# Performance work log

Hardware: AMD Instinct MI355X
Metric: run time of the kernel (lower is better)

## Reference

```python
import jax, jax.numpy as jnp
import numpy as np
from jax import lax

DIM = 128
DEPTH = 2
OUT_DIM = 256
DIM_HEAD = 64
HEADS = 8
WS = 16
INNER = DIM_HEAD * HEADS
EPS = 1e-5
SCALE = DIM_HEAD ** (-0.5)


def setup_inputs() -> dict:
    key = jax.random.key(0)
    ks = jax.random.split(key, 20)
    s = 0.02
    L = DEPTH
    inp = {
        "x": jax.random.normal(ks[0], (1, DIM, 256, 256), dtype=jnp.float32),
        "ln1_g": jnp.ones((L, DIM), dtype=jnp.float32),
        "ln1_b": jnp.zeros((L, DIM), dtype=jnp.float32),
        "wq": jax.random.normal(ks[1], (L, INNER, DIM), dtype=jnp.float32) * s,
        "wkv": jax.random.normal(ks[2], (L, 2 * INNER, DIM), dtype=jnp.float32) * s,
        "wo": jax.random.normal(ks[3], (L, DIM, INNER), dtype=jnp.float32) * s,
        "bo": jnp.zeros((L, DIM), dtype=jnp.float32),
        "ln2_g": jnp.ones((L, DIM), dtype=jnp.float32),
        "ln2_b": jnp.zeros((L, DIM), dtype=jnp.float32),
        "w_in": jax.random.normal(ks[4], (L, DIM, DIM), dtype=jnp.float32) * s,
        "b_in": jnp.zeros((L, DIM), dtype=jnp.float32),
        "w_c3": jax.random.normal(ks[5], (L, OUT_DIM, DIM, 3, 3), dtype=jnp.float32) * s,
        "b_c3": jnp.zeros((L, OUT_DIM), dtype=jnp.float32),
        "w_c1": jax.random.normal(ks[6], (L, DIM, OUT_DIM), dtype=jnp.float32) * s,
        "b_c1": jnp.zeros((L, DIM), dtype=jnp.float32),
        "w_outer": jax.random.normal(ks[7], (DIM, DIM), dtype=jnp.float32) * s,
        "b_outer": jnp.zeros((DIM,), dtype=jnp.float32),
    }
    return inp


def _layernorm(x, g, b):
    # channel-wise (dim=1) norm; note torch code uses (std + eps), not sqrt(var + eps)
    mean = jnp.mean(x, axis=1, keepdims=True)
    std = jnp.sqrt(jnp.var(x, axis=1, keepdims=True))
    return (x - mean) / (std + EPS) * g[None, :, None, None] + b[None, :, None, None]


def _conv1x1(w, x, b=None):
    y = jnp.einsum('oi,bihw->bohw', w, x)
    if b is not None:
        y = y + b[None, :, None, None]
    return y


def _to_windows(t, B, H, W):
    # [B, HEADS*DIM_HEAD, H, W] -> [B*HEADS*nx*ny, WS*WS, DIM_HEAD]
    nx, ny = H // WS, W // WS
    t = t.reshape(B, HEADS, DIM_HEAD, nx, WS, ny, WS)
    t = t.transpose(0, 1, 3, 5, 4, 6, 2)
    return t.reshape(B * HEADS * nx * ny, WS * WS, DIM_HEAD)


def _from_windows(t, B, H, W):
    nx, ny = H // WS, W // WS
    t = t.reshape(B, HEADS, nx, ny, WS, WS, DIM_HEAD)
    t = t.transpose(0, 1, 6, 2, 4, 3, 5)
    return t.reshape(B, HEADS * DIM_HEAD, H, W)


def _attention(x, wq_l, wkv_l, wo_l, bo_l):
    B, _, H, W = x.shape
    q = _conv1x1(wq_l, x)
    kv = _conv1x1(wkv_l, x)
    k, v = kv[:, :INNER], kv[:, INNER:]
    q = _to_windows(q, B, H, W)
    k = _to_windows(k, B, H, W)
    v = _to_windows(v, B, H, W)
    sim = jnp.einsum('bid,bjd->bij', q, k) * SCALE  # [nwin, 256, 256]
    attn = jax.nn.softmax(sim, axis=-1)
    out = jnp.einsum('bij,bjd->bid', attn, v)
    out = _from_windows(out, B, H, W)
    return _conv1x1(wo_l, out, bo_l)


def _feedforward(x, w_in_l, b_in_l, w_c3_l, b_c3_l, w_c1_l, b_c1_l):
    h = _conv1x1(w_in_l, x, b_in_l)
    h = lax.conv_general_dilated(h, w_c3_l, window_strides=(1, 1), padding='SAME',
                                 dimension_numbers=('NCHW', 'OIHW', 'NCHW'))
    h = h + b_c3_l[None, :, None, None]
    h = jax.nn.gelu(h, approximate=False)
    return _conv1x1(w_c1_l, h, b_c1_l)


def reference(x, ln1_g, ln1_b, wq, wkv, wo, bo, ln2_g, ln2_b,
              w_in, b_in, w_c3, b_c3, w_c1, b_c1, w_outer, b_outer):
    for l in range(DEPTH):
        xn = _layernorm(x, ln1_g[l], ln1_b[l])
        x = _attention(xn, wq[l], wkv[l], wo[l], bo[l]) + x
        xn = _layernorm(x, ln2_g[l], ln2_b[l])
        x = _feedforward(xn, w_in[l], b_in[l], w_c3[l], b_c3[l], w_c1[l], b_c1[l]) + x
    return _conv1x1(w_outer, x, b_outer) + x
```

## Files before the change

kernel.cpp:

```cpp
#include <hip/hip_runtime.h>
#include <hip/hip_bf16.h>
#include <math.h>

typedef __hip_bfloat16 bf16;
typedef float f4 __attribute__((ext_vector_type(4)));
typedef short s8 __attribute__((ext_vector_type(8)));
typedef unsigned int u2 __attribute__((ext_vector_type(2)));
typedef unsigned int u4v __attribute__((ext_vector_type(4)));

__device__ __forceinline__ void gload16(const void* g, char* l) {
  __builtin_amdgcn_global_load_lds(
      (const __attribute__((address_space(1))) unsigned int*)g,
      (__attribute__((address_space(3))) unsigned int*)l, 16, 0, 0);
}
__device__ __forceinline__ unsigned short bfr(float f) {
  bf16 h = __float2bfloat16(f);
  return *(unsigned short*)&h;
}
__device__ __forceinline__ unsigned int pk2(float a, float b) {
  return (unsigned int)bfr(a) | ((unsigned int)bfr(b) << 16);
}
__device__ __forceinline__ unsigned int pkt(float a, float b) {
  return __builtin_amdgcn_perm(__float_as_uint(b), __float_as_uint(a), 0x07060302u);
}

__global__ __launch_bounds__(256) void prep_w(
    const float* __restrict__ wq, const float* __restrict__ wkv,
    const float* __restrict__ wo, const float* __restrict__ win,
    const float* __restrict__ wc3, const float* __restrict__ wc1,
    const float* __restrict__ wout, ushort* __restrict__ cw)
{
  int i = blockIdx.x * 256 + threadIdx.x;
  float v;
  if (i < 131072) v = wq[i];
  else if (i < 393216) v = wkv[i - 131072];
  else if (i < 524288) v = wo[i - 393216];
  else if (i < 1146880) return;
  else if (i < 1212416) v = wc1[i - 1146880];
  else if (i < 1228800) v = wout[i - 1212416];
  else if (i < 1230848) { cw[i] = 0; return; }
  else return;
  cw[i] = bfr(v);
}

__global__ __launch_bounds__(128) void prep_fold(
    const float* __restrict__ wc3, const float* __restrict__ win,
    const float* __restrict__ b_in, ushort* __restrict__ cw3out,
    float* __restrict__ T)
{
  __shared__ float col[128][9];
  __shared__ float sred[2][9];
  const int lyr = blockIdx.x >> 8, m = blockIdx.x & 255;
  const int tid = threadIdx.x;
  const float* src = wc3 + (((size_t)lyr * 256 + m) * 128 + tid) * 9;
#pragma unroll
  for (int t = 0; t < 9; ++t) col[tid][t] = src[t];
  float bi = b_in[lyr * 128 + tid];
  float sb[9];
#pragma unroll
  for (int t = 0; t < 9; ++t) {
    float v = col[tid][t] * bi;
    v += __shfl_xor(v, 1, 64);  v += __shfl_xor(v, 2, 64);
    v += __shfl_xor(v, 4, 64);  v += __shfl_xor(v, 8, 64);
    v += __shfl_xor(v, 16, 64); v += __shfl_xor(v, 32, 64);
    sb[t] = v;
  }
  if ((tid & 63) == 0) {
#pragma unroll
    for (int t = 0; t < 9; ++t) sred[tid >> 6][t] = sb[t];
  }
  __syncthreads();
  float acc[9] = {0.f,0.f,0.f,0.f,0.f,0.f,0.f,0.f,0.f};
  const float* wrow = win + (size_t)lyr * 16384 + tid;
  for (int c = 0; c < 128; ++c) {
    float wv = wrow[(size_t)c * 128];
#pragma unroll
    for (int t = 0; t < 9; ++t) acc[t] += col[c][t] * wv;
  }
  ushort* dst = cw3out + (size_t)lyr * 294912 + (size_t)m * 1152 + tid;
#pragma unroll
  for (int t = 0; t < 9; ++t) dst[t * 128] = bfr(acc[t]);
  if (tid == 0) {
    float s[9];
#pragma unroll
    for (int t = 0; t < 9; ++t) s[t] = sred[0][t] + sred[1][t];
    float* Tl = T + lyr * 2304;
    Tl[0 * 256 + m] = s[0]+s[1]+s[2]+s[3]+s[4]+s[5]+s[6]+s[7]+s[8];
    Tl[1 * 256 + m] = s[0] + s[1] + s[2];
    Tl[2 * 256 + m] = s[6] + s[7] + s[8];
    Tl[3 * 256 + m] = s[0] + s[3] + s[6];
    Tl[4 * 256 + m] = s[2] + s[5] + s[8];
    Tl[5 * 256 + m] = s[0];
    Tl[6 * 256 + m] = s[2];
    Tl[7 * 256 + m] = s[6];
    Tl[8 * 256 + m] = s[8];
  }
}

template<bool NCHW>
__global__ __launch_bounds__(256) void ln_nhwc(
    const float* __restrict__ x, const float* __restrict__ g,
    const float* __restrict__ b, ushort* __restrict__ y)
{
  const int p = blockIdx.x * 256 + threadIdx.x;
  f4 v[32];
  float s = 0.f, s2 = 0.f;
  if constexpr (NCHW) {
#pragma unroll
    for (int i = 0; i < 32; ++i)
#pragma unroll
      for (int j = 0; j < 4; ++j) {
        float t = x[(size_t)(i * 4 + j) * 65536 + p];
        v[i][j] = t; s += t; s2 += t * t;
      }
  } else {
    const f4* base = (const f4*)(x + (size_t)p * 128);
#pragma unroll
    for (int i = 0; i < 32; ++i) {
      v[i] = base[i];
#pragma unroll
      for (int j = 0; j < 4; ++j) { s += v[i][j]; s2 += v[i][j] * v[i][j]; }
    }
  }
  float mean = s * (1.f / 128.f);
  float var = s2 * (1.f / 128.f) - mean * mean;
  var = var > 0.f ? var : 0.f;
  float inv = 1.f / (sqrtf(var) + 1e-5f);
  u2* dst = (u2*)(y + (size_t)p * 128);
#pragma unroll
  for (int i = 0; i < 32; ++i) {
    f4 gg = *(const f4*)(g + i * 4);
    f4 bb = *(const f4*)(b + i * 4);
    float f0 = (v[i][0] - mean) * inv * gg[0] + bb[0];
    float f1 = (v[i][1] - mean) * inv * gg[1] + bb[1];
    float f2 = (v[i][2] - mean) * inv * gg[2] + bb[2];
    float f3 = (v[i][3] - mean) * inv * gg[3] + bb[3];
    u2 st; st.x = pk2(f0, f1); st.y = pk2(f2, f3);
    dst[i] = st;
  }
}

template<int MODE>
__global__ __launch_bounds__(256) void gemm_nhwc(
    const ushort* __restrict__ A, const ushort* __restrict__ X,
    const float* __restrict__ bias, const float* __restrict__ res,
    void* __restrict__ out, ushort* __restrict__ out2,
    const ushort* __restrict__ A2,
    const float* __restrict__ lng, const float* __restrict__ lnb,
    ushort* __restrict__ xn, const int K, const int M)
{
  constexpr unsigned SMSZ = (MODE == 7) ? 65536u : 32768u;
  __shared__ __align__(16) char sm[SMSZ];
  const int tid = threadIdx.x, w = tid >> 6, l = tid & 63;
  const int quad = l >> 4, l15 = l & 15;
  const int n0 = blockIdx.x * 128, m0 = blockIdx.y * 128;
  const int mh = (w & 1) * 64, nh = (w >> 1) * 64;
  const f4 fz = {0.f, 0.f, 0.f, 0.f};
  f4 acc[4][4];
#pragma unroll
  for (int a = 0; a < 4; ++a)
#pragma unroll
    for (int b2 = 0; b2 < 4; ++b2) acc[a][b2] = fz;

  const int KI = K >> 6;
  for (int kk = 0; kk < KI; ++kk) {
    if (kk) __syncthreads();
    const int k0 = kk << 6;
#pragma unroll
    for (int j = 0; j < 4; ++j) {
      int p = j * 256 + tid, r = p >> 3, c = (p & 7) ^ (r & 7);
      gload16(A + (size_t)(m0 + r) * K + k0 + c * 8, sm + (j * 256 + w * 64) * 16);
    }
#pragma unroll
    for (int j = 0; j < 4; ++j) {
      int p = j * 256 + tid, r = p >> 3, c = (p & 7) ^ (r & 7);
      gload16(X + (size_t)(n0 + r) * K + k0 + c * 8, sm + 16384 + (j * 256 + w * 64) * 16);
    }
    __syncthreads();
#pragma unroll
    for (int ks = 0; ks < 2; ++ks) {
      s8 af[4], bx[4];
#pragma unroll
      for (int mt = 0; mt < 4; ++mt) {
        int rr = mh + mt * 16 + l15;
        af[mt] = *(const s8*)(sm + rr * 128 + (((ks * 4 + quad) ^ (rr & 7)) << 4));
      }
#pragma unroll
      for (int nt = 0; nt < 4; ++nt) {
        int rr = nh + nt * 16 + l15;
        bx[nt] = *(const s8*)(sm + 16384 + rr * 128 + (((ks * 4 + quad) ^ (rr & 7)) << 4));
      }
#pragma unroll
      for (int mt = 0; mt < 4; ++mt)
#pragma unroll
        for (int nt = 0; nt < 4; ++nt)
          acc[mt][nt] = __builtin_amdgcn_mfma_f32_16x16x32_bf16(af[mt], bx[nt], acc[mt][nt], 0, 0, 0);
    }
  }

  if constexpr (MODE == 7) {
#pragma unroll
    for (int mt = 0; mt < 4; ++mt) {
      const int m = mh + mt * 16 + quad * 4;
      f4 bb = *(const f4*)(bias + m);
      const int seg = m >> 6, kl = m & 63;
#pragma unroll
      for (int nt = 0; nt < 4; ++nt) {
        const int r = nh + nt * 16 + l15;
        f4 v = acc[mt][nt] + bb + *(const f4*)(res + (size_t)(n0 + r) * 128 + m);
        acc[mt][nt] = v;
        u2 st; st.x = pk2(v[0], v[1]); st.y = pk2(v[2], v[3]);
        *(u2*)(sm + 32768 + seg * 16384 + r * 128 +
               (((kl >> 3) ^ (r & 7)) << 4) + (kl & 7) * 2) = st;
      }
    }
    __syncthreads();
#pragma unroll
    for (int kk2 = 0; kk2 < 2; ++kk2)
#pragma unroll
      for (int j = 0; j < 4; ++j) {
        int p = j * 256 + tid, r = p >> 3, c = (p & 7) ^ (r & 7);
        gload16(A2 + (size_t)r * 128 + kk2 * 64 + c * 8,
                sm + kk2 * 16384 + (j * 256 + w * 64) * 16);
      }
    __syncthreads();
    f4 acc2[4][4];
#pragma unroll
    for (int a = 0; a < 4; ++a)
#pragma unroll
      for (int b2 = 0; b2 < 4; ++b2) acc2[a][b2] = fz;
#pragma unroll
    for (int kk2 = 0; kk2 < 2; ++kk2)
#pragma unroll
      for (int ks = 0; ks < 2; ++ks) {
        s8 af[4], bx[4];
#pragma unroll
        for (int mt = 0; mt < 4; ++mt) {
          int rr = mh + mt * 16 + l15;
          af[mt] = *(const s8*)(sm + kk2 * 16384 + rr * 128 + (((ks * 4 + quad) ^ (rr & 7)) << 4));
        }
#pragma unroll
        for (int nt = 0; nt < 4; ++nt) {
          int rr = nh + nt * 16 + l15;
          bx[nt] = *(const s8*)(sm + 32768 + kk2 * 16384 + rr * 128 + (((ks * 4 + quad) ^ (rr & 7)) << 4));
        }
#pragma unroll
        for (int mt = 0; mt < 4; ++mt)
#pragma unroll
          for (int nt = 0; nt < 4; ++nt)
            acc2[mt][nt] = __builtin_amdgcn_mfma_f32_16x16x32_bf16(af[mt], bx[nt], acc2[mt][nt], 0, 0, 0);
      }
#pragma unroll
    for (int mt = 0; mt < 4; ++mt) {
      const int m = mh + mt * 16 + quad * 4;
      f4 bo2 = *(const f4*)(lng + m);
#pragma unroll
      for (int nt = 0; nt < 4; ++nt) {
        const int n = n0 + nh + nt * 16 + l15;
        f4 v2 = acc2[mt][nt] + bo2 + acc[mt][nt];
#pragma unroll
        for (int i = 0; i < 4; ++i)
          ((float*)out)[(size_t)(m + i) * 65536 + n] = v2[i];
      }
    }
    return;
  }

  if constexpr (MODE == 5 || MODE == 6) {
    float s1[4] = {0.f, 0.f, 0.f, 0.f}, s2[4] = {0.f, 0.f, 0.f, 0.f};
#pragma unroll
    for (int mt = 0; mt < 4; ++mt) {
      const int m = mh + mt * 16 + quad * 4;
      f4 bb = *(const f4*)(bias + m);
#pragma unroll
      for (int nt = 0; nt < 4; ++nt) {
        const int n = n0 + nh + nt * 16 + l15;
        f4 v = acc[mt][nt] + bb;
        if constexpr (MODE == 5) {
          f4 r = *(const f4*)(res + (size_t)n * 128 + m);
          v += r;
        } else {
          f4 r;
#pragma unroll
          for (int i = 0; i < 4; ++i) r[i] = res[(size_t)(m + i) * 65536 + n];
          v += r;
        }
        *(f4*)((float*)out + (size_t)n * 128 + m) = v;
        acc[mt][nt] = v;
        s1[nt] += v[0] + v[1] + v[2] + v[3];
        s2[nt] += v[0] * v[0] + v[1] * v[1] + v[2] * v[2] + v[3] * v[3];
      }
    }
    __syncthreads();
    float* pb = (float*)sm;
#pragma unroll
    for (int nt = 0; nt < 4; ++nt) {
      float a1 = s1[nt], a2 = s2[nt];
      a1 += __shfl_xor(a1, 16, 64); a1 += __shfl_xor(a1, 32, 64);
      a2 += __shfl_xor(a2, 16, 64); a2 += __shfl_xor(a2, 32, 64);
      s1[nt] = a1; s2[nt] = a2;
      if (quad == 0) {
        int pn = nh + nt * 16 + l15;
        pb[((w & 1) * 128 + pn) * 2]     = a1;
        pb[((w & 1) * 128 + pn) * 2 + 1] = a2;
      }
    }
    __syncthreads();
#pragma unroll
    for (int nt = 0; nt < 4; ++nt) {
      int pn = nh + nt * 16 + l15;
      float t1 = s1[nt] + pb[((1 - (w & 1)) * 128 + pn) * 2];
      float t2 = s2[nt] + pb[((1 - (w & 1)) * 128 + pn) * 2 + 1];
      float mean = t1 * (1.f / 128.f);
      float var = t2 * (1.f / 128.f) - mean * mean;
      var = var > 0.f ? var : 0.f;
      s1[nt] = mean;
      s2[nt] = 1.f / (sqrtf(var) + 1e-5f);
    }
#pragma unroll
    for (int mt = 0; mt < 4; ++mt) {
      const int m = mh + mt * 16 + quad * 4;
      f4 gg = *(const f4*)(lng + m);
      f4 b2 = *(const f4*)(lnb + m);
#pragma unroll
      for (int nt = 0; nt < 4; ++nt) {
        const int n = n0 + nh + nt * 16 + l15;
        f4 v = acc[mt][nt];
        float mean = s1[nt], inv = s2[nt];
        float f0 = (v[0] - mean) * inv * gg[0] + b2[0];
        float f1 = (v[1] - mean) * inv * gg[1] + b2[1];
        float f2 = (v[2] - mean) * inv * gg[2] + b2[2];
        float f3 = (v[3] - mean) * inv * gg[3] + b2[3];
        u2 st; st.x = pk2(f0, f1); st.y = pk2(f2, f3);
        *(u2*)(xn + (size_t)n * 128 + m) = st;
      }
    }
    return;
  }

#pragma unroll
  for (int mt = 0; mt < 4; ++mt) {
#pragma unroll
    for (int nt = 0; nt < 4; ++nt) {
      const int m = m0 + mh + mt * 16 + quad * 4;
      const int n = n0 + nh + nt * 16 + l15;
      f4 bb = *(const f4*)(bias + m);
      f4 v = acc[mt][nt] + bb;
      if constexpr (MODE == 0) {
        u2 st; st.x = pk2(v[0], v[1]); st.y = pk2(v[2], v[3]);
        *(u2*)((ushort*)out + (size_t)n * M + m) = st;
      } else if constexpr (MODE == 1 || MODE == 3) {
        f4 r = *(const f4*)(res + (size_t)n * M + m);
        v += r;
        *(f4*)((float*)out + (size_t)n * M + m) = v;
        if constexpr (MODE == 3) {
          u2 st; st.x = pk2(v[0], v[1]); st.y = pk2(v[2], v[3]);
          *(u2*)(out2 + (size_t)n * M + m) = st;
        }
      } else if constexpr (MODE == 4) {
        f4 r;
#pragma unroll
        for (int i = 0; i < 4; ++i) r[i] = res[(size_t)(m + i) * 65536 + n];
        v += r;
        *(f4*)((float*)out + (size_t)n * M + m) = v;
      } else {
        f4 r = *(const f4*)(res + (size_t)n * M + m);
#pragma unroll
        for (int i = 0; i < 4; ++i)
          ((float*)out)[(size_t)(m + i) * 65536 + n] = v[i] + r[i];
      }
    }
  }
}

__global__ __launch_bounds__(256) void conv3_kernel(
    const ushort* __restrict__ A, const ushort* __restrict__ X,
    const float* __restrict__ bias, ushort* __restrict__ out,
    const ushort* __restrict__ zp, const float* __restrict__ T)
{
  __shared__ __align__(16) char sm[32768];
  const int tid = threadIdx.x, w = tid >> 6, l = tid & 63;
  const int quad = l >> 4, l15 = l & 15;
  const int n0 = blockIdx.x * 128, m0 = blockIdx.y * 128;
  const int mh = (w & 1) * 64, nh = (w >> 1) * 64;
  const f4 fz = {0.f, 0.f, 0.f, 0.f};
  f4 acc[4][4];
#pragma unroll
  for (int a = 0; a < 4; ++a)
#pragma unroll
    for (int b2 = 0; b2 < 4; ++b2) acc[a][b2] = fz;

  for (int kk = 0; kk < 18; ++kk) {
    if (kk) __syncthreads();
    const int tap = kk >> 1, ky = tap / 3, kx = tap - ky * 3;
    const int dn = (ky - 1) * 256 + (kx - 1);
    const int kseg = (kk & 1) << 6;
#pragma unroll
    for (int j = 0; j < 4; ++j) {
      int p = j * 256 + tid, r = p >> 3, c = (p & 7) ^ (r & 7);
      gload16(A + (size_t)(m0 + r) * 1152 + kk * 64 + c * 8, sm + (j * 256 + w * 64) * 16);
    }
#pragma unroll
    for (int j = 0; j < 4; ++j) {
      int p = j * 256 + tid, r = p >> 3, c = (p & 7) ^ (r & 7);
      int nl = n0 + r;
      int ys = (nl >> 8) + ky - 1, xs = (nl & 255) + kx - 1;
      const ushort* gp = ((unsigned)ys < 256u && (unsigned)xs < 256u)
                         ? X + (size_t)(nl + dn) * 128 + kseg + c * 8 : zp;
      gload16(gp, sm + 16384 + (j * 256 + w * 64) * 16);
    }
    __syncthreads();
#pragma unroll
    for (int ks = 0; ks < 2; ++ks) {
      s8 af[4], bx[4];
#pragma unroll
      for (int mt = 0; mt < 4; ++mt) {
        int rr = mh + mt * 16 + l15;
        af[mt] = *(const s8*)(sm + rr * 128 + (((ks * 4 + quad) ^ (rr & 7)) << 4));
      }
#pragma unroll
      for (int nt = 0; nt < 4; ++nt) {
        int rr = nh + nt * 16 + l15;
        bx[nt] = *(const s8*)(sm + 16384 + rr * 128 + (((ks * 4 + quad) ^ (rr & 7)) << 4));
      }
#pragma unroll
      for (int mt = 0; mt < 4; ++mt)
#pragma unroll
        for (int nt = 0; nt < 4; ++nt)
          acc[mt][nt] = __builtin_amdgcn_mfma_f32_16x16x32_bf16(af[mt], bx[nt], acc[mt][nt], 0, 0, 0);
    }
  }
  const int y = n0 >> 8;
  const bool y0 = (y == 0), y1 = (y == 255);
  const int xbase = (n0 & 255) + nh;
#pragma unroll
  for (int mt = 0; mt < 4; ++mt) {
    const int m = m0 + mh + mt * 16 + quad * 4;
    f4 base = *(const f4*)(bias + m) + *(const f4*)(T + m);
    f4 Lc = *(const f4*)(T + 3 * 256 + m);
    f4 Rc = *(const f4*)(T + 4 * 256 + m);
    if (y0) {
      base -= *(const f4*)(T + 1 * 256 + m);
      Lc -= *(const f4*)(T + 5 * 256 + m);
      Rc -= *(const f4*)(T + 6 * 256 + m);
    }
    if (y1) {
      base -= *(const f4*)(T + 2 * 256 + m);
      Lc -= *(const f4*)(T + 7 * 256 + m);
      Rc -= *(const f4*)(T + 8 * 256 + m);
    }
#pragma unroll
    for (int nt = 0; nt < 4; ++nt) {
      const int n = n0 + nh + nt * 16 + l15;
      const int x = xbase + nt * 16 + l15;
      float fx0 = (x == 0) ? 1.f : 0.f;
      float fx1 = (x == 255) ? 1.f : 0.f;
      f4 v = acc[mt][nt] + base - Lc * fx0 - Rc * fx1;
      float g0 = 0.5f * v[0] * (1.f + erff(v[0] * 0.70710678118f));
      float g1 = 0.5f * v[1] * (1.f + erff(v[1] * 0.70710678118f));
      float g2 = 0.5f * v[2] * (1.f + erff(v[2] * 0.70710678118f));
      float g3 = 0.5f * v[3] * (1.f + erff(v[3] * 0.70710678118f));
      u2 st; st.x = pk2(g0, g1); st.y = pk2(g2, g3);
      *(u2*)(out + (size_t)n * 256 + m) = st;
    }
  }
}

__global__ __launch_bounds__(1024) void attn_kernel(
    const ushort* __restrict__ xn, const ushort* __restrict__ wq,
    const ushort* __restrict__ wkv, ushort* __restrict__ ao)
{
  __shared__ __align__(16) char sm[147456];
  const int tid = threadIdx.x, w = tid >> 6, l = tid & 63;
  const int quad = l >> 4, l15 = l & 15;
  const int win = blockIdx.x, head = blockIdx.y;
  const int nbase = ((win >> 4) << 12) + ((win & 15) << 4);
  char* RX  = sm;
  char* RW  = sm + 65536;
  char* RK  = sm + 114688;
  char* RVT = sm;
  char* Pw  = sm + 32768 + w * 2048;
  char* RO  = RW;
  const f4 fz = {0.f, 0.f, 0.f, 0.f};
  const int tokw = w * 16 + l15;

#pragma unroll
  for (int j = 0; j < 4; ++j) {
    int p = j * 1024 + tid, r = p >> 4, c = (p & 15) ^ (r & 15);
    int n = nbase + ((r >> 4) << 8) + (r & 15);
    gload16(xn + (size_t)n * 128 + c * 8, RX + (j * 1024 + w * 64) * 16);
  }
  {
    const ushort* wpq = wq + (size_t)head * 64 * 128;
    const ushort* wpk = wkv + (size_t)head * 64 * 128;
    const ushort* wpv = wkv + (size_t)(512 + head * 64) * 128;
    int r = tid >> 4, c = (tid & 15) ^ (r & 15);
    gload16(wpq + (size_t)r * 128 + c * 8, RW + w * 1024);
    gload16(wpk + (size_t)r * 128 + c * 8, RW + 16384 + w * 1024);
    gload16(wpv + (size_t)r * 128 + c * 8, RW + 32768 + w * 1024);
  }
  __syncthreads();

  s8 bq[2];
  {
    f4 acc[4];
#pragma unroll
    for (int a = 0; a < 4; ++a) acc[a] = fz;
#pragma unroll
    for (int ks = 0; ks < 4; ++ks) {
      s8 af[4], bx;
#pragma unroll
      for (int mt = 0; mt < 4; ++mt) {
        int rr = mt * 16 + l15;
        af[mt] = *(const s8*)(RW + rr * 256 + (((ks * 4 + quad) ^ (rr & 15)) << 4));
      }
      bx = *(const s8*)(RX + tokw * 256 + (((ks * 4 + quad) ^ (tokw & 15)) << 4));
#pragma unroll
      for (int mt = 0; mt < 4; ++mt)
        acc[mt] = __builtin_amdgcn_mfma_f32_16x16x32_bf16(af[mt], bx, acc[mt], 0, 0, 0);
    }
    unsigned pd[4][2];
#pragma unroll
    for (int mt = 0; mt < 4; ++mt) {
      pd[mt][0] = pkt(acc[mt][0], acc[mt][1]);
      pd[mt][1] = pkt(acc[mt][2], acc[mt][3]);
    }
#pragma unroll
    for (int ks = 0; ks < 2; ++ks) {
      u4v t;
#pragma unroll
      for (int dj = 0; dj < 4; ++dj) {
        int srcl = l15 + (((quad & 1) * 2 + (dj >> 1)) << 4);
        unsigned va = (unsigned)__shfl((int)pd[2 * ks][dj & 1], srcl, 64);
        unsigned vb = (unsigned)__shfl((int)pd[2 * ks + 1][dj & 1], srcl, 64);
        t[dj] = (quad < 2) ? va : vb;
      }
      bq[ks] = __builtin_bit_cast(s8, t);
    }
  }

  {
    f4 acc[4];
#pragma unroll
    for (int a = 0; a < 4; ++a) acc[a] = fz;
#pragma unroll
    for (int ks = 0; ks < 4; ++ks) {
      s8 af[4], bx;
#pragma unroll
      for (int mt = 0; mt < 4; ++mt) {
        int rr = mt * 16 + l15;
        af[mt] = *(const s8*)(RW + 16384 + rr * 256 + (((ks * 4 + quad) ^ (rr & 15)) << 4));
      }
      bx = *(const s8*)(RX + tokw * 256 + (((ks * 4 + quad) ^ (tokw & 15)) << 4));
#pragma unroll
      for (int mt = 0; mt < 4; ++mt)
        acc[mt] = __builtin_amdgcn_mfma_f32_16x16x32_bf16(af[mt], bx, acc[mt], 0, 0, 0);
    }
#pragma unroll
    for (int mt = 0; mt < 4; ++mt) {
      int d0 = mt * 16 + quad * 4;
      char* a = RK + tokw * 128 + (((d0 >> 3) ^ (tokw & 7)) << 4) + (d0 & 7) * 2;
      *(unsigned int*)a = pkt(acc[mt][0], acc[mt][1]);
      *(unsigned int*)(a + 4) = pkt(acc[mt][2], acc[mt][3]);
    }
  }

  {
    f4 acc[4];
#pragma unroll
    for (int a = 0; a < 4; ++a) acc[a] = fz;
#pragma unroll
    for (int ks = 0; ks < 4; ++ks) {
      s8 ax, bw[4];
      ax = *(const s8*)(RX + tokw * 256 + (((ks * 4 + quad) ^ (tokw & 15)) << 4));
#pragma unroll
      for (int nt = 0; nt < 4; ++nt) {
        int rr = nt * 16 + l15;
        bw[nt] = *(const s8*)(RW + 32768 + rr * 256 + (((ks * 4 + quad) ^ (rr & 15)) << 4));
      }
#pragma unroll
      for (int nt = 0; nt < 4; ++nt)
        acc[nt] = __builtin_amdgcn_mfma_f32_16x16x32_bf16(ax, bw[nt], acc[nt], 0, 0, 0);
    }
    __syncthreads();
#pragma unroll
    for (int nt = 0; nt < 4; ++nt) {
      int d = nt * 16 + l15, t0 = w * 16 + quad * 4;
      char* a = RVT + d * 512 + (((t0 >> 3) ^ (d & 31)) << 4) + (t0 & 7) * 2;
      *(unsigned int*)a = pkt(acc[nt][0], acc[nt][1]);
      *(unsigned int*)(a + 4) = pkt(acc[nt][2], acc[nt][3]);
    }
  }
  __syncthreads();

  f4 o[4];
  float lsum = 0.f;
#pragma unroll
  for (int a = 0; a < 4; ++a) o[a] = fz;

  for (int jt = 0; jt < 4; ++jt) {
    f4 s[4];
#pragma unroll
    for (int a = 0; a < 4; ++a) s[a] = fz;
#pragma unroll
    for (int ks = 0; ks < 2; ++ks) {
      s8 af[4];
#pragma unroll
      for (int mt = 0; mt < 4; ++mt) {
        int rr = jt * 64 + mt * 16 + l15;
        af[mt] = *(const s8*)(RK + rr * 128 + (((ks * 4 + quad) ^ (rr & 7)) << 4));
      }
      __builtin_amdgcn_s_setprio(1);
#pragma unroll
      for (int mt = 0; mt < 4; ++mt)
        s[mt] = __builtin_amdgcn_mfma_f32_16x16x32_bf16(af[mt], bq[ks], s[mt], 0, 0, 0);
      __builtin_amdgcn_s_setprio(0);
    }
#pragma unroll
    for (int mt = 0; mt < 4; ++mt) {
      float p0 = exp2f(s[mt][0] * 0.18033688f);
      float p1 = exp2f(s[mt][1] * 0.18033688f);
      float p2 = exp2f(s[mt][2] * 0.18033688f);
      float p3 = exp2f(s[mt][3] * 0.18033688f);
      lsum += p0 + p1 + p2 + p3;
      int j0 = mt * 16 + quad * 4;
      char* a = Pw + l15 * 128 + (((j0 >> 3) ^ (l15 & 7)) << 4) + (j0 & 7) * 2;
      *(unsigned int*)a = pkt(p0, p1);
      *(unsigned int*)(a + 4) = pkt(p2, p3);
    }
#pragma unroll
    for (int ks = 0; ks < 2; ++ks) {
      s8 av[4], bp;
#pragma unroll
      for (int mt = 0; mt < 4; ++mt) {
        int d = mt * 16 + l15;
        av[mt] = *(const s8*)(RVT + d * 512 + (((jt * 8 + ks * 4 + quad) ^ (d & 31)) << 4));
      }
      bp = *(const s8*)(Pw + l15 * 128 + (((ks * 4 + quad) ^ (l15 & 7)) << 4));
      __builtin_amdgcn_s_setprio(1);
#pragma unroll
      for (int mt = 0; mt < 4; ++mt)
        o[mt] = __builtin_amdgcn_mfma_f32_16x16x32_bf16(av[mt], bp, o[mt], 0, 0, 0);
      __builtin_amdgcn_s_setprio(0);
    }
  }

  float lv = lsum;
  lv += __shfl_xor(lv, 16, 64);
  lv += __shfl_xor(lv, 32, 64);
  const float inv = 1.f / lv;
#pragma unroll
  for (int mt = 0; mt < 4; ++mt) {
    int i = w * 16 + l15, d0 = mt * 16 + quad * 4;
    char* a = RO + i * 128 + (((d0 >> 3) ^ (i & 7)) << 4) + (d0 & 7) * 2;
    *(unsigned int*)a = pkt(o[mt][0] * inv, o[mt][1] * inv);
    *(unsigned int*)(a + 4) = pkt(o[mt][2] * inv, o[mt][3] * inv);
  }
  __syncthreads();
  const int tok = tid >> 2, q2 = tid & 3;
  const int n = nbase + ((tok >> 4) << 8) + (tok & 15);
  ushort* dst = ao + (size_t)n * 512 + head * 64;
#pragma unroll
  for (int c = 0; c < 2; ++c) {
    int chunk = q2 * 2 + c;
    u4v v = *(const u4v*)(RO + tok * 128 + ((chunk ^ (tok & 7)) << 4));
    *(u4v*)(dst + chunk * 8) = v;
  }
}

extern "C" void kernel_launch(void* const* d_in, const int* in_sizes, int n_in,
                              void* d_out, int out_size, void* d_ws, size_t ws_size,
                              hipStream_t stream)
{
  const float* x_in    = (const float*)d_in[0];
  const float* ln1_g   = (const float*)d_in[1];
  const float* ln1_b   = (const float*)d_in[2];
  const float* wq      = (const float*)d_in[3];
  const float* wkv     = (const float*)d_in[4];
  const float* wo      = (const float*)d_in[5];
  const float* bo      = (const float*)d_in[6];
  const float* ln2_g   = (const float*)d_in[7];
  const float* ln2_b   = (const float*)d_in[8];
  const float* w_in    = (const float*)d_in[9];
  const float* b_in    = (const float*)d_in[10];
  const float* w_c3    = (const float*)d_in[11];
  const float* b_c3    = (const float*)d_in[12];
  const float* w_c1    = (const float*)d_in[13];
  const float* b_c1    = (const float*)d_in[14];
  const float* w_outer = (const float*)d_in[15];
  const float* b_outer = (const float*)d_in[16];

  char* wsb = (char*)d_ws;
  ushort* CW = (ushort*)wsb;
  float*  TB = (float*)(wsb + 3145728);
  float*  XH = (float*)(wsb + 4194304);
  ushort* XN = (ushort*)(wsb + 37748736);
  ushort* AO = (ushort*)(wsb + 54525952);
  ushort* G  = (ushort*)(wsb + 138412032);

  const ushort* zp = CW + 1228800;
  dim3 b256(256);

  prep_w<<<dim3(4808), b256, 0, stream>>>(wq, wkv, wo, w_in, w_c3, w_c1, w_outer, CW);
  prep_fold<<<dim3(512), dim3(128), 0, stream>>>(w_c3, w_in, b_in, CW + 557056, TB);

  ln_nhwc<true><<<dim3(256), b256, 0, stream>>>(x_in, ln1_g, ln1_b, XN);
  attn_kernel<<<dim3(256, 8), dim3(1024), 0, stream>>>(XN, CW, CW + 131072, AO);
  gemm_nhwc<6><<<dim3(512, 1), b256, 0, stream>>>(CW + 393216, AO, bo, x_in, XH,
      nullptr, nullptr, ln2_g, ln2_b, XN, 512, 128);
  conv3_kernel<<<dim3(512, 2), b256, 0, stream>>>(CW + 557056, XN, b_c3, G, zp, TB);
  gemm_nhwc<5><<<dim3(512, 1), b256, 0, stream>>>(CW + 1146880, G, b_c1, XH, XH,
      nullptr, nullptr, ln1_g + 128, ln1_b + 128, XN, 256, 128);

  attn_kernel<<<dim3(256, 8), dim3(1024), 0, stream>>>(XN, CW + 65536, CW + 262144, AO);
  gemm_nhwc<5><<<dim3(512, 1), b256, 0, stream>>>(CW + 458752, AO, bo + 128, XH, XH,
      nullptr, nullptr, ln2_g + 128, ln2_b + 128, XN, 512, 128);
  conv3_kernel<<<dim3(512, 2), b256, 0, stream>>>(CW + 851968, XN, b_c3 + 256, G, zp, TB + 2304);
  gemm_nhwc<7><<<dim3(512, 1), b256, 0, stream>>>(CW + 1179648, G, b_c1 + 128, XH, d_out,
      nullptr, CW + 1212416, b_outer, nullptr, nullptr, 256, 128);
}
```

Measured before the change: 648.4 us.

## Load attention operands straight from global into registers and shrink LDS footprint

The attention kernel no longer stages the window activations and the Q/K/V weight slices through shared memory. Each wave loads its own token fragments and the weight fragments directly from global memory into MFMA operand registers. The P matrix is also passed to the PV MFMA through lane shuffles instead of a per-wave LDS scratch. This cuts shared memory from 144KB to 64KB, removes a barrier, and may allow more blocks per CU, at the cost of redundant uncoalesced weight reads from global/L2 by every wave and extra shuffle instructions.

```diff
diff --git a/kernel.cpp b/kernel.cpp
--- a/kernel.cpp
+++ b/kernel.cpp
@@ -470,36 +470,26 @@
     const ushort* __restrict__ xn, const ushort* __restrict__ wq,
     const ushort* __restrict__ wkv, ushort* __restrict__ ao)
 {
-  __shared__ __align__(16) char sm[147456];
+  __shared__ __align__(16) char sm[65536];
   const int tid = threadIdx.x, w = tid >> 6, l = tid & 63;
   const int quad = l >> 4, l15 = l & 15;
   const int win = blockIdx.x, head = blockIdx.y;
   const int nbase = ((win >> 4) << 12) + ((win & 15) << 4);
-  char* RX  = sm;
-  char* RW  = sm + 65536;
-  char* RK  = sm + 114688;
-  char* RVT = sm;
-  char* Pw  = sm + 32768 + w * 2048;
-  char* RO  = RW;
+  char* RK  = sm;
+  char* RVT = sm + 32768;
+  char* RO  = sm;
   const f4 fz = {0.f, 0.f, 0.f, 0.f};
   const int tokw = w * 16 + l15;
 
-#pragma unroll
-  for (int j = 0; j < 4; ++j) {
-    int p = j * 1024 + tid, r = p >> 4, c = (p & 15) ^ (r & 15);
-    int n = nbase + ((r >> 4) << 8) + (r & 15);
-    gload16(xn + (size_t)n * 128 + c * 8, RX + (j * 1024 + w * 64) * 16);
-  }
-  {
-    const ushort* wpq = wq + (size_t)head * 64 * 128;
-    const ushort* wpk = wkv + (size_t)head * 64 * 128;
-    const ushort* wpv = wkv + (size_t)(512 + head * 64) * 128;
-    int r = tid >> 4, c = (tid & 15) ^ (r & 15);
-    gload16(wpq + (size_t)r * 128 + c * 8, RW + w * 1024);
-    gload16(wpk + (size_t)r * 128 + c * 8, RW + 16384 + w * 1024);
-    gload16(wpv + (size_t)r * 128 + c * 8, RW + 32768 + w * 1024);
-  }
-  __syncthreads();
+  const size_t xrow = (size_t)(nbase + w * 256 + l15) * 128;
+  s8 xf[4];
+#pragma unroll
+  for (int ks = 0; ks < 4; ++ks)
+    xf[ks] = *(const s8*)(xn + xrow + (ks * 4 + quad) * 8);
+
+  const ushort* wpq = wq + (size_t)head * 64 * 128;
+  const ushort* wpk = wkv + (size_t)head * 64 * 128;
+  const ushort* wpv = wkv + (size_t)(512 + head * 64) * 128;
 
   s8 bq[2];
   {
@@ -508,16 +498,13 @@
     for (int a = 0; a < 4; ++a) acc[a] = fz;
 #pragma unroll
     for (int ks = 0; ks < 4; ++ks) {
-      s8 af[4], bx;
-#pragma unroll
-      for (int mt = 0; mt < 4; ++mt) {
-        int rr = mt * 16 + l15;
-        af[mt] = *(const s8*)(RW + rr * 256 + (((ks * 4 + quad) ^ (rr & 15)) << 4));
-      }
-      bx = *(const s8*)(RX + tokw * 256 + (((ks * 4 + quad) ^ (tokw & 15)) << 4));
+      s8 af[4];
 #pragma unroll
       for (int mt = 0; mt < 4; ++mt)
-        acc[mt] = __builtin_amdgcn_mfma_f32_16x16x32_bf16(af[mt], bx, acc[mt], 0, 0, 0);
+        af[mt] = *(const s8*)(wpq + (size_t)(mt * 16 + l15) * 128 + (ks * 4 + quad) * 8);
+#pragma unroll
+      for (int mt = 0; mt < 4; ++mt)
+        acc[mt] = __builtin_amdgcn_mfma_f32_16x16x32_bf16(af[mt], xf[ks], acc[mt], 0, 0, 0);
     }
     unsigned pd[4][2];
 #pragma unroll
@@ -545,16 +532,13 @@
     for (int a = 0; a < 4; ++a) acc[a] = fz;
 #pragma unroll
     for (int ks = 0; ks < 4; ++ks) {
-      s8 af[4], bx;
-#pragma unroll
-      for (int mt = 0; mt < 4; ++mt) {
-        int rr = mt * 16 + l15;
-        af[mt] = *(const s8*)(RW + 16384 + rr * 256 + (((ks * 4 + quad) ^ (rr & 15)) << 4));
-      }
-      bx = *(const s8*)(RX + tokw * 256 + (((ks * 4 + quad) ^ (tokw & 15)) << 4));
+      s8 af[4];
 #pragma unroll
       for (int mt = 0; mt < 4; ++mt)
-        acc[mt] = __builtin_amdgcn_mfma_f32_16x16x32_bf16(af[mt], bx, acc[mt], 0, 0, 0);
+        af[mt] = *(const s8*)(wpk + (size_t)(mt * 16 + l15) * 128 + (ks * 4 + quad) * 8);
+#pragma unroll
+      for (int mt = 0; mt < 4; ++mt)
+        acc[mt] = __builtin_amdgcn_mfma_f32_16x16x32_bf16(af[mt], xf[ks], acc[mt], 0, 0, 0);
     }
 #pragma unroll
     for (int mt = 0; mt < 4; ++mt) {
@@ -571,18 +555,14 @@
     for (int a = 0; a < 4; ++a) acc[a] = fz;
 #pragma unroll
     for (int ks = 0; ks < 4; ++ks) {
-      s8 ax, bw[4];
-      ax = *(const s8*)(RX + tokw * 256 + (((ks * 4 + quad) ^ (tokw & 15)) << 4));
-#pragma unroll
-      for (int nt = 0; nt < 4; ++nt) {
-        int rr = nt * 16 + l15;
-        bw[nt] = *(const s8*)(RW + 32768 + rr * 256 + (((ks * 4 + quad) ^ (rr & 15)) << 4));
-      }
+      s8 bw[4];
 #pragma unroll
       for (int nt = 0; nt < 4; ++nt)
-        acc[nt] = __builtin_amdgcn_mfma_f32_16x16x32_bf16(ax, bw[nt], acc[nt], 0, 0, 0);
-    }
-    __syncthreads();
+        bw[nt] = *(const s8*)(wpv + (size_t)(nt * 16 + l15) * 128 + (ks * 4 + quad) * 8);
+#pragma unroll
+      for (int nt = 0; nt < 4; ++nt)
+        acc[nt] = __builtin_amdgcn_mfma_f32_16x16x32_bf16(xf[ks], bw[nt], acc[nt], 0, 0, 0);
+    }
 #pragma unroll
     for (int nt = 0; nt < 4; ++nt) {
       int d = nt * 16 + l15, t0 = w * 16 + quad * 4;
@@ -616,31 +596,44 @@
         s[mt] = __builtin_amdgcn_mfma_f32_16x16x32_bf16(af[mt], bq[ks], s[mt], 0, 0, 0);
       __builtin_amdgcn_s_setprio(0);
     }
-#pragma unroll
-    for (int mt = 0; mt < 4; ++mt) {
-      float p0 = exp2f(s[mt][0] * 0.18033688f);
-      float p1 = exp2f(s[mt][1] * 0.18033688f);
-      float p2 = exp2f(s[mt][2] * 0.18033688f);
-      float p3 = exp2f(s[mt][3] * 0.18033688f);
-      lsum += p0 + p1 + p2 + p3;
-      int j0 = mt * 16 + quad * 4;
-      char* a = Pw + l15 * 128 + (((j0 >> 3) ^ (l15 & 7)) << 4) + (j0 & 7) * 2;
-      *(unsigned int*)a = pkt(p0, p1);
-      *(unsigned int*)(a + 4) = pkt(p2, p3);
+    s8 bp[2];
+    {
+      unsigned pd[4][2];
+#pragma unroll
+      for (int mt = 0; mt < 4; ++mt) {
+        float p0 = exp2f(s[mt][0] * 0.18033688f);
+        float p1 = exp2f(s[mt][1] * 0.18033688f);
+        float p2 = exp2f(s[mt][2] * 0.18033688f);
+        float p3 = exp2f(s[mt][3] * 0.18033688f);
+        lsum += p0 + p1 + p2 + p3;
+        pd[mt][0] = pkt(p0, p1);
+        pd[mt][1] = pkt(p2, p3);
+      }
+#pragma unroll
+      for (int ks = 0; ks < 2; ++ks) {
+        u4v t;
+#pragma unroll
+        for (int dj = 0; dj < 4; ++dj) {
+          int srcl = l15 + (((quad & 1) * 2 + (dj >> 1)) << 4);
+          unsigned va = (unsigned)__shfl((int)pd[2 * ks][dj & 1], srcl, 64);
+          unsigned vb = (unsigned)__shfl((int)pd[2 * ks + 1][dj & 1], srcl, 64);
+          t[dj] = (quad < 2) ? va : vb;
+        }
+        bp[ks] = __builtin_bit_cast(s8, t);
+      }
     }
 #pragma unroll
     for (int ks = 0; ks < 2; ++ks) {
-      s8 av[4], bp;
+      s8 av[4];
 #pragma unroll
       for (int mt = 0; mt < 4; ++mt) {
         int d = mt * 16 + l15;
         av[mt] = *(const s8*)(RVT + d * 512 + (((jt * 8 + ks * 4 + quad) ^ (d & 31)) << 4));
       }
-      bp = *(const s8*)(Pw + l15 * 128 + (((ks * 4 + quad) ^ (l15 & 7)) << 4));
       __builtin_amdgcn_s_setprio(1);
 #pragma unroll
       for (int mt = 0; mt < 4; ++mt)
-        o[mt] = __builtin_amdgcn_mfma_f32_16x16x32_bf16(av[mt], bp, o[mt], 0, 0, 0);
+        o[mt] = __builtin_amdgcn_mfma_f32_16x16x32_bf16(av[mt], bp[ks], o[mt], 0, 0, 0);
       __builtin_amdgcn_s_setprio(0);
     }
   }
@@ -649,6 +642,7 @@
   lv += __shfl_xor(lv, 16, 64);
   lv += __shfl_xor(lv, 32, 64);
   const float inv = 1.f / lv;
+  __syncthreads();
 #pragma unroll
   for (int mt = 0; mt < 4; ++mt) {
     int i = w * 16 + l15, d0 = mt * 16 + quad * 4;
```

After: 861.1 us. 1.33x slower.
